# Kernel tuning notes

Measured on AMD Instinct MI355X. Metric: run time of the kernel, lower is better.

Reference implementation:

```python
import jax, jax.numpy as jnp
import numpy as np

N, M, D = 8192, 8192, 64
P = 2            # Wasserstein order (geomloss p=2 -> cost = |x-y|^2 / 2)
BLUR = 0.05      # entropic blur
SCALING = 0.5    # epsilon-scaling ratio
DIAMETER = 32.0  # conservative static diameter bound for randn data (jit-static schedule)


def _eps_schedule():
    # geomloss epsilon_schedule: eps anneals from diameter^p down to blur^p by scaling^p
    eps_list = [DIAMETER ** P]
    e = DIAMETER
    while e > BLUR:
        e = max(e * SCALING, BLUR)
        eps_list.append(e ** P)
    return eps_list

EPS_LIST = _eps_schedule()


def _sqdist(x, y):
    # (N,M) pairwise squared euclidean distances, clamped for numerical safety
    x2 = jnp.sum(x * x, axis=1)[:, None]
    y2 = jnp.sum(y * y, axis=1)[None, :]
    return jnp.maximum(x2 + y2 - 2.0 * (x @ y.T), 0.0)


def _softmin(eps, C, h_log):
    # softmin_eps over columns: -eps * logsumexp_j( h_log[j] - C[i,j]/eps )
    return -eps * jax.nn.logsumexp(h_log[None, :] - C / eps, axis=1)


def _sinkhorn_divergence(x, y):
    n, m = x.shape[0], y.shape[0]
    a_log = jnp.full((n,), -float(np.log(n)), dtype=x.dtype)  # uniform log-weights
    b_log = jnp.full((m,), -float(np.log(m)), dtype=x.dtype)

    C_xy = 0.5 * _sqdist(x, y)   # p=2 geomloss cost
    C_yx = C_xy.T
    C_xx = 0.5 * _sqdist(x, x)
    C_yy = 0.5 * _sqdist(y, y)

    eps0 = EPS_LIST[0]
    f_aa = _softmin(eps0, C_xx, a_log)   # symmetric self potential on x
    g_bb = _softmin(eps0, C_yy, b_log)   # symmetric self potential on y
    g_ab = _softmin(eps0, C_yx, a_log)   # potential on y from alpha
    f_ba = _softmin(eps0, C_xy, b_log)   # potential on x from beta

    # epsilon-scaling Sinkhorn loop with symmetric (averaged) updates
    for eps in EPS_LIST:
        ft = _softmin(eps, C_xy, b_log + g_ab / eps)
        gt = _softmin(eps, C_yx, a_log + f_ba / eps)
        fs = _softmin(eps, C_xx, a_log + f_aa / eps)
        gs = _softmin(eps, C_yy, b_log + g_bb / eps)
        f_ba, g_ab = 0.5 * (f_ba + ft), 0.5 * (g_ab + gt)
        f_aa, g_bb = 0.5 * (f_aa + fs), 0.5 * (g_bb + gs)

    # final non-averaged extrapolation at eps = blur^p
    eps = EPS_LIST[-1]
    f_ba_f = _softmin(eps, C_xy, b_log + g_ab / eps)
    g_ab_f = _softmin(eps, C_yx, a_log + f_ba / eps)
    f_aa_f = _softmin(eps, C_xx, a_log + f_aa / eps)
    g_bb_f = _softmin(eps, C_yy, b_log + g_bb / eps)

    # debiased Sinkhorn divergence: <a, f-f_aa> + <b, g-g_bb> (uniform weights)
    return jnp.mean(f_ba_f - f_aa_f) + jnp.mean(g_ab_f - g_bb_f)


def setup_inputs() -> dict:
    key = jax.random.key(0)
    k1, k2 = jax.random.split(key)
    return {
        "pred_signature": jax.random.normal(k1, (N, D), dtype=jnp.float32),
        "target_signature": jax.random.normal(k2, (M, D), dtype=jnp.float32),
    }


def reference(pred_signature, target_signature):
    # distances is a single scalar (one point-cloud pair); .mean() is identity
    x = pred_signature.astype(jnp.float32)
    y = target_signature.astype(jnp.float32)
    return _sinkhorn_divergence(x, y)
```

## Files before the change

kernel.cpp:

```cpp
#include <hip/hip_runtime.h>
#include <math.h>

#define NPTS 8192
#define DIM  64
#define NCH  4
#define JCH  2048
#define NRB  64
#define JT   16
#define LSYH 72
#define NPART 8

static const float LN2_ = 0.69314718055994530942f;

typedef _Float16 f16x8 __attribute__((ext_vector_type(8)));
typedef float    f32x4 __attribute__((ext_vector_type(4)));

__device__ __forceinline__ float fexp2(float x) {
#if __has_builtin(__builtin_amdgcn_exp2f)
    return __builtin_amdgcn_exp2f(x);
#else
    return exp2f(x);
#endif
}

__global__ void norms_kernel(const float* __restrict__ x, const float* __restrict__ y,
                             float* __restrict__ x2h, float* __restrict__ y2h) {
    int i = blockIdx.x * blockDim.x + threadIdx.x;
    const float* src = (i < NPTS) ? x : y;
    float* dst = (i < NPTS) ? x2h : y2h;
    int r = (i < NPTS) ? i : i - NPTS;
    const float4* p = (const float4*)(src + (size_t)r * DIM);
    float s = 0.f;
#pragma unroll
    for (int k = 0; k < DIM / 4; ++k) {
        float4 v = p[k];
        s += v.x * v.x + v.y * v.y + v.z * v.z + v.w * v.w;
    }
    dst[r] = 0.5f * s;
}

__global__ void convert_kernel(const float* __restrict__ x, const float* __restrict__ y,
                               _Float16* __restrict__ xh, _Float16* __restrict__ yh) {
    int i = blockIdx.x * 256 + threadIdx.x;
    int e = i * 8;
    const float* src; _Float16* dst; int off;
    if (e < NPTS * DIM) { src = x; dst = xh; off = e; }
    else                { src = y; dst = yh; off = e - NPTS * DIM; }
    float4 a = *(const float4*)(src + off);
    float4 b = *(const float4*)(src + off + 4);
    f16x8 o = { (_Float16)a.x, (_Float16)a.y, (_Float16)a.z, (_Float16)a.w,
                (_Float16)b.x, (_Float16)b.y, (_Float16)b.z, (_Float16)b.w };
    *(f16x8*)(dst + off) = o;
}

__launch_bounds__(256, 3)
__global__ void softmin_kernel(const _Float16* __restrict__ xh, const _Float16* __restrict__ yh,
                               const float* __restrict__ x2h, const float* __restrict__ y2h,
                               const float* __restrict__ g_ab, const float* __restrict__ f_ba,
                               const float* __restrict__ f_aa, const float* __restrict__ g_bb,
                               float* __restrict__ partials,
                               float inv_eps, int use_g) {
    const int jb = blockIdx.y;
    const int rb = blockIdx.x / NCH;
    const int ch = blockIdx.x % NCH;

    const _Float16* X; const _Float16* Y; const float* g; const float* ynorm;
    if (jb == 0)      { X = xh; Y = yh; g = g_ab; ynorm = y2h; }
    else if (jb == 1) { X = yh; Y = xh; g = f_ba; ynorm = x2h; }
    else if (jb == 2) { X = xh; Y = xh; g = f_aa; ynorm = x2h; }
    else              { X = yh; Y = yh; g = g_bb; ynorm = y2h; }

    __shared__ _Float16 ys[128 * LSYH];
    __shared__ float hys[JCH];

    const int t = threadIdx.x;
    const int wave = t >> 6, lane = t & 63;
    const int wr = wave >> 1, wc = wave & 1;
    const int l15 = lane & 15, quad = lane >> 4;

    const float base = -9.0109131783f;
    const float L2E  = 1.44269504089f;
    const float inv2 = inv_eps * L2E;

    for (int j = t; j < JCH; j += 256) {
        int jj = ch * JCH + j;
        float hl = base;
        if (use_g) hl += g[jj] * inv_eps;
        hys[j] = L2E * hl - ynorm[jj] * inv2;
    }

    const int i0 = rb * 128 + wr * 64;
    f16x8 af[4][2];
#pragma unroll
    for (int u = 0; u < 4; ++u)
#pragma unroll
        for (int h = 0; h < 2; ++h)
            af[u][h] = *(const f16x8*)(X + ((size_t)(i0 + u * 16 + l15)) * DIM + h * 32 + quad * 8);

    const int srow = t >> 3, skc = t & 7;
    f16x8 pre[4];
#pragma unroll
    for (int c = 0; c < 4; ++c)
        pre[c] = *(const f16x8*)(Y + ((size_t)ch * JCH + (srow + c * 32)) * DIM + skc * 8);

    float m[16], s[16];
#pragma unroll
    for (int u = 0; u < 16; ++u) { m[u] = -3.0e38f; s[u] = 0.f; }

    for (int jt = 0; jt < JT; ++jt) {
        __syncthreads();
#pragma unroll
        for (int c = 0; c < 4; ++c)
            *(f16x8*)&ys[(srow + c * 32) * LSYH + skc * 8] = pre[c];
        __syncthreads();

        {
            int jn = (jt + 1 < JT) ? jt + 1 : jt;
            const _Float16* srcY = Y + ((size_t)ch * JCH + (size_t)jn * 128) * DIM;
#pragma unroll
            for (int c = 0; c < 4; ++c)
                pre[c] = *(const f16x8*)(srcY + (srow + c * 32) * DIM + skc * 8);
        }

        f16x8 bf[4][2];
#pragma unroll
        for (int v = 0; v < 4; ++v)
#pragma unroll
            for (int h = 0; h < 2; ++h)
                bf[v][h] = *(const f16x8*)&ys[(wc * 64 + v * 16 + l15) * LSYH + h * 32 + quad * 8];

        float hvv[4];
#pragma unroll
        for (int v = 0; v < 4; ++v)
            hvv[v] = hys[jt * 128 + wc * 64 + v * 16 + l15];

#pragma unroll
        for (int u = 0; u < 4; ++u) {
            f32x4 acc[4];
#pragma unroll
            for (int v = 0; v < 4; ++v) {
                f32x4 z = {0.f, 0.f, 0.f, 0.f};
                z = __builtin_amdgcn_mfma_f32_16x16x32_f16(af[u][0], bf[v][0], z, 0, 0, 0);
                acc[v] = __builtin_amdgcn_mfma_f32_16x16x32_f16(af[u][1], bf[v][1], z, 0, 0, 0);
            }
#pragma unroll
            for (int r = 0; r < 4; ++r) {
                int idx = u * 4 + r;
                float w0 = fmaf(acc[0][r], inv2, hvv[0]);
                float w1 = fmaf(acc[1][r], inv2, hvv[1]);
                float w2 = fmaf(acc[2][r], inv2, hvv[2]);
                float w3 = fmaf(acc[3][r], inv2, hvv[3]);
                float mn = fmaxf(fmaxf(fmaxf(w0, w1), fmaxf(w2, w3)), m[idx]);
                float e0 = fexp2(w0 - mn), e1 = fexp2(w1 - mn);
                float e2 = fexp2(w2 - mn), e3 = fexp2(w3 - mn);
                s[idx] = fmaf(s[idx], fexp2(m[idx] - mn), (e0 + e1) + (e2 + e3));
                m[idx] = mn;
            }
        }
    }

#pragma unroll
    for (int st = 1; st <= 8; st <<= 1) {
#pragma unroll
        for (int u = 0; u < 16; ++u) {
            float mo = __shfl_xor(m[u], st, 64);
            float so = __shfl_xor(s[u], st, 64);
            float M = fmaxf(m[u], mo);
            s[u] = s[u] * fexp2(m[u] - M) + so * fexp2(mo - M);
            m[u] = M;
        }
    }
    if (l15 == 0) {
        int p = ch * 2 + wc;
#pragma unroll
        for (int u = 0; u < 4; ++u)
#pragma unroll
            for (int r = 0; r < 4; ++r) {
                int row = i0 + u * 16 + quad * 4 + r;
                size_t off = (((size_t)jb * NPART + p) * NPTS + row) * 2;
                partials[off]     = m[u * 4 + r];
                partials[off + 1] = s[u * 4 + r];
            }
    }
}

__global__ void combine_kernel(const float* __restrict__ partials,
                               const float* __restrict__ x2h, const float* __restrict__ y2h,
                               float* __restrict__ o0, float* __restrict__ o1,
                               float* __restrict__ o2, float* __restrict__ o3,
                               float eps, int avg) {
    int jb = blockIdx.y;
    int i = blockIdx.x * 256 + threadIdx.x;
    const float* xn = (jb == 0 || jb == 2) ? x2h : y2h;
    float* out = (jb == 0) ? o0 : (jb == 1) ? o1 : (jb == 2) ? o2 : o3;

    float mv[NPART], sv[NPART];
    float M = -3.0e38f;
#pragma unroll
    for (int p = 0; p < NPART; ++p) {
        size_t off = (((size_t)jb * NPART + p) * NPTS + i) * 2;
        mv[p] = partials[off];
        sv[p] = partials[off + 1];
        M = fmaxf(M, mv[p]);
    }
    float st = 0.f;
#pragma unroll
    for (int p = 0; p < NPART; ++p) st += sv[p] * fexp2(mv[p] - M);
    float val = xn[i] - eps * LN2_ * (M + __log2f(st));
    if (avg) val = 0.5f * (out[i] + val);
    out[i] = val;
}

__global__ void reduce_kernel(const float* __restrict__ fba, const float* __restrict__ gab,
                              const float* __restrict__ faa, const float* __restrict__ gbb,
                              float* __restrict__ out) {
    __shared__ float red[256];
    int t = threadIdx.x;
    float s = 0.f;
    for (int i = t; i < NPTS; i += 256)
        s += (fba[i] - faa[i]) + (gab[i] - gbb[i]);
    red[t] = s;
    __syncthreads();
    for (int st = 128; st > 0; st >>= 1) {
        if (t < st) red[t] += red[t + st];
        __syncthreads();
    }
    if (t == 0) out[0] = red[0] / (float)NPTS;
}

extern "C" void kernel_launch(void* const* d_in, const int* in_sizes, int n_in,
                              void* d_out, int out_size, void* d_ws, size_t ws_size,
                              hipStream_t stream) {
    const float* x = (const float*)d_in[0];
    const float* y = (const float*)d_in[1];
    float* ws = (float*)d_ws;

    float* x2h   = ws + 0 * NPTS;
    float* y2h   = ws + 1 * NPTS;
    float* f_ba  = ws + 2 * NPTS;
    float* g_ab  = ws + 3 * NPTS;
    float* f_aa  = ws + 4 * NPTS;
    float* g_bb  = ws + 5 * NPTS;
    float* fba_f = ws + 6 * NPTS;
    float* gab_f = ws + 7 * NPTS;
    float* faa_f = ws + 8 * NPTS;
    float* gbb_f = ws + 9 * NPTS;
    float* partials = ws + 10 * NPTS;
    _Float16* xh = (_Float16*)(ws + 74 * NPTS);
    _Float16* yh = xh + (size_t)NPTS * DIM;

    const float EPS[11] = {1024.f, 256.f, 64.f, 16.f, 4.f, 1.f,
                           0.25f, 0.0625f, 0.015625f, 0.00390625f, 0.0025f};

    norms_kernel<<<dim3(2 * NPTS / 256), dim3(256), 0, stream>>>(x, y, x2h, y2h);
    convert_kernel<<<dim3(2 * NPTS * DIM / 8 / 256), dim3(256), 0, stream>>>(x, y, xh, yh);

    dim3 sgrid(NRB * NCH, 4), sblk(256);
    dim3 cgrid(NPTS / 256, 4), cblk(256);

    softmin_kernel<<<sgrid, sblk, 0, stream>>>(xh, yh, x2h, y2h, g_ab, f_ba, f_aa, g_bb,
                                               partials, 1.f / EPS[0], 0);
    combine_kernel<<<cgrid, cblk, 0, stream>>>(partials, x2h, y2h,
                                               f_ba, g_ab, f_aa, g_bb, EPS[0], 0);

    for (int it = 0; it < 11; ++it) {
        softmin_kernel<<<sgrid, sblk, 0, stream>>>(xh, yh, x2h, y2h, g_ab, f_ba, f_aa, g_bb,
                                                   partials, 1.f / EPS[it], 1);
        combine_kernel<<<cgrid, cblk, 0, stream>>>(partials, x2h, y2h,
                                                   f_ba, g_ab, f_aa, g_bb, EPS[it], 1);
    }

    softmin_kernel<<<sgrid, sblk, 0, stream>>>(xh, yh, x2h, y2h, g_ab, f_ba, f_aa, g_bb,
                                               partials, 1.f / EPS[10], 1);
    combine_kernel<<<cgrid, cblk, 0, stream>>>(partials, x2h, y2h,
                                               fba_f, gab_f, faa_f, gbb_f, EPS[10], 0);

    reduce_kernel<<<1, 256, 0, stream>>>(fba_f, gab_f, faa_f, gbb_f, (float*)d_out);
}
```

Measured before the change: 1.015 ms.

## Split column range into three padded chunks and skip negligible exp updates

The column dimension is now split into three chunks of 2731 instead of four of 2048. The last tile is padded with -inf bias and clamped row loads, which changes the grid size and the partial count. The online logsumexp update is also skipped when a group's max is more than 40 log2 units below the running max. That drops exp work that would contribute nothing, at the cost of a divergent branch and some padded wasted tiles.

New measurement: 1.176 ms. +15.9%, slower.

```diff
diff --git a/kernel.cpp b/kernel.cpp
--- a/kernel.cpp
+++ b/kernel.cpp
@@ -3,12 +3,13 @@
 
 #define NPTS 8192
 #define DIM  64
-#define NCH  4
-#define JCH  2048
+#define NCH  3
+#define CW   2731
+#define JPAD 2816
+#define JTP  22
 #define NRB  64
-#define JT   16
 #define LSYH 72
-#define NPART 8
+#define NPART 6
 
 static const float LN2_ = 0.69314718055994530942f;
 
@@ -71,7 +72,7 @@
     else              { X = yh; Y = yh; g = g_bb; ynorm = y2h; }
 
     __shared__ _Float16 ys[128 * LSYH];
-    __shared__ float hys[JCH];
+    __shared__ float hys[JPAD];
 
     const int t = threadIdx.x;
     const int wave = t >> 6, lane = t & 63;
@@ -82,11 +83,18 @@
     const float L2E  = 1.44269504089f;
     const float inv2 = inv_eps * L2E;
 
-    for (int j = t; j < JCH; j += 256) {
-        int jj = ch * JCH + j;
-        float hl = base;
-        if (use_g) hl += g[jj] * inv_eps;
-        hys[j] = L2E * hl - ynorm[jj] * inv2;
+    const int cstart = ch * CW;
+    const int clen   = (ch == 2) ? (NPTS - 2 * CW) : CW;
+
+    for (int j = t; j < JPAD; j += 256) {
+        float hv = -3.0e38f;
+        if (j < clen) {
+            int jj = cstart + j;
+            float hl = base;
+            if (use_g) hl += g[jj] * inv_eps;
+            hv = L2E * hl - ynorm[jj] * inv2;
+        }
+        hys[j] = hv;
     }
 
     const int i0 = rb * 128 + wr * 64;
@@ -100,14 +108,17 @@
     const int srow = t >> 3, skc = t & 7;
     f16x8 pre[4];
 #pragma unroll
-    for (int c = 0; c < 4; ++c)
-        pre[c] = *(const f16x8*)(Y + ((size_t)ch * JCH + (srow + c * 32)) * DIM + skc * 8);
+    for (int c = 0; c < 4; ++c) {
+        int jr = cstart + srow + c * 32;
+        jr = (jr < NPTS) ? jr : (NPTS - 1);
+        pre[c] = *(const f16x8*)(Y + (size_t)jr * DIM + skc * 8);
+    }
 
     float m[16], s[16];
 #pragma unroll
     for (int u = 0; u < 16; ++u) { m[u] = -3.0e38f; s[u] = 0.f; }
 
-    for (int jt = 0; jt < JT; ++jt) {
+    for (int jt = 0; jt < JTP; ++jt) {
         __syncthreads();
 #pragma unroll
         for (int c = 0; c < 4; ++c)
@@ -115,11 +126,13 @@
         __syncthreads();
 
         {
-            int jn = (jt + 1 < JT) ? jt + 1 : jt;
-            const _Float16* srcY = Y + ((size_t)ch * JCH + (size_t)jn * 128) * DIM;
-#pragma unroll
-            for (int c = 0; c < 4; ++c)
-                pre[c] = *(const f16x8*)(srcY + (srow + c * 32) * DIM + skc * 8);
+            int jn = (jt + 1 < JTP) ? jt + 1 : jt;
+#pragma unroll
+            for (int c = 0; c < 4; ++c) {
+                int jr = cstart + jn * 128 + srow + c * 32;
+                jr = (jr < NPTS) ? jr : (NPTS - 1);
+                pre[c] = *(const f16x8*)(Y + (size_t)jr * DIM + skc * 8);
+            }
         }
 
         f16x8 bf[4][2];
@@ -150,11 +163,14 @@
                 float w1 = fmaf(acc[1][r], inv2, hvv[1]);
                 float w2 = fmaf(acc[2][r], inv2, hvv[2]);
                 float w3 = fmaf(acc[3][r], inv2, hvv[3]);
-                float mn = fmaxf(fmaxf(fmaxf(w0, w1), fmaxf(w2, w3)), m[idx]);
-                float e0 = fexp2(w0 - mn), e1 = fexp2(w1 - mn);
-                float e2 = fexp2(w2 - mn), e3 = fexp2(w3 - mn);
-                s[idx] = fmaf(s[idx], fexp2(m[idx] - mn), (e0 + e1) + (e2 + e3));
-                m[idx] = mn;
+                float wm = fmaxf(fmaxf(w0, w1), fmaxf(w2, w3));
+                if (wm >= m[idx] - 40.0f) {
+                    float mn = fmaxf(m[idx], wm);
+                    float e0 = fexp2(w0 - mn), e1 = fexp2(w1 - mn);
+                    float e2 = fexp2(w2 - mn), e3 = fexp2(w3 - mn);
+                    s[idx] = fmaf(s[idx], fexp2(m[idx] - mn), (e0 + e1) + (e2 + e3));
+                    m[idx] = mn;
+                }
             }
         }
     }
```
